# Performance work log

Measured on AMD Instinct MI355X. Metric: run time of the kernel, lower is better.

The kernel has to match this reference:

```python
import jax, jax.numpy as jnp
import numpy as np

B, N, E, H, D = 64, 500, 128, 8, 16  # batch, pomo==graph size, embed, heads, qkv_dim
NEG = -1e9
LOGIT_CLIP = 10.0


def setup_inputs() -> dict:
    key = jax.random.key(0)
    ks = jax.random.split(key, 10)
    enc_nodes = jax.random.normal(ks[0], (B, N, E), dtype=jnp.float32)
    enc_first = jax.random.normal(ks[1], (B, N, E), dtype=jnp.float32)
    enc_last = jax.random.normal(ks[2], (B, N, E), dtype=jnp.float32)
    mask_bits = jax.random.uniform(ks[3], (B, N, N)) < 0.2
    ninf_mask = jnp.where(mask_bits, jnp.float32(NEG), jnp.float32(0.0))
    # Linear weights (torch layout [out_features, in_features])
    sc = 1.0 / np.sqrt(E)
    Wq_first = jax.random.normal(ks[4], (H * D, E), dtype=jnp.float32) * sc
    Wq_last = jax.random.normal(ks[5], (H * D, E), dtype=jnp.float32) * sc
    Wk = jax.random.normal(ks[6], (H * D, E), dtype=jnp.float32) * sc
    Wv = jax.random.normal(ks[7], (H * D, E), dtype=jnp.float32) * sc
    Wc = jax.random.normal(ks[8], (E, H * D), dtype=jnp.float32) / np.sqrt(H * D)
    bc = jax.random.normal(ks[9], (E,), dtype=jnp.float32) * 0.01
    return {"encoded_nodes": enc_nodes, "encoded_first_node": enc_first,
            "encoded_last_node": enc_last, "ninf_mask": ninf_mask,
            "Wq_first": Wq_first, "Wq_last": Wq_last, "Wk": Wk, "Wv": Wv,
            "Wc": Wc, "bc": bc}


def _heads(x, W):
    # x: [B, n, E], W: [H*D, E] -> [B, H, n, D]
    y = jnp.einsum('bne,fe->bnf', x, W)
    return y.reshape(x.shape[0], x.shape[1], H, D).transpose(0, 2, 1, 3)


def reference(encoded_nodes, encoded_first_node, encoded_last_node, ninf_mask,
              Wq_first, Wq_last, Wk, Wv, Wc, bc):
    # set_q1 + Wq_last projection, summed per POMO decoder
    q = _heads(encoded_first_node, Wq_first) + _heads(encoded_last_node, Wq_last)  # [B,H,N,D]
    k = _heads(encoded_nodes, Wk)  # [B,H,N,D]
    v = _heads(encoded_nodes, Wv)  # [B,H,N,D]
    # masked multi-head attention
    score = jnp.einsum('bhnd,bhgd->bhng', q, k) / jnp.sqrt(jnp.float32(D))
    score = score + ninf_mask[:, None, :, :]
    w = jax.nn.softmax(score, axis=-1)
    out = jnp.einsum('bhng,bhgd->bhnd', w, v)  # [B,H,N,D]
    out_concat = out.transpose(0, 2, 1, 3).reshape(B, N, H * D)
    mh = jnp.einsum('bnf,ef->bne', out_concat, Wc) + bc  # multi_head_combine
    # single-head pointer attention with tanh clipping
    s = jnp.einsum('bne,bge->bng', mh, encoded_nodes) / jnp.sqrt(jnp.float32(E))
    s = LOGIT_CLIP * jnp.tanh(s) + ninf_mask
    probs = jax.nn.softmax(s, axis=2)
    return probs
```

## Files before the change

kernel.cpp:

```cpp
#include <hip/hip_runtime.h>


#define B_ 64
#define N_ 500

typedef short bf16x8 __attribute__((ext_vector_type(8)));
typedef float f32x16 __attribute__((ext_vector_type(16)));
typedef unsigned short ushort8 __attribute__((ext_vector_type(8)));

__device__ __forceinline__ float4 ld4(const float* p) { return *reinterpret_cast<const float4*>(p); }
__device__ __forceinline__ void st4(float* p, const float4 v) { *reinterpret_cast<float4*>(p) = v; }

__device__ __forceinline__ float fast_tanh(float x) {
    const float e = __expf(2.f * x);
    return 1.f - 2.f / (e + 1.f);
}

__device__ __forceinline__ unsigned short f2bf_rn(float x) {
    unsigned u = __float_as_uint(x);
    return (unsigned short)((u + 0x7FFFu + ((u >> 16) & 1u)) >> 16);
}
__device__ __forceinline__ float bf2f(unsigned short h) {
    return __uint_as_float(((unsigned)h) << 16);
}

__global__ __launch_bounds__(256) void gemm_mfma(
    const float* __restrict__ A1, const float* __restrict__ W1a, const float* __restrict__ W1b,
    const float* __restrict__ A2, const float* __restrict__ W2a, const float* __restrict__ W2b,
    const float* __restrict__ bias, float* __restrict__ C, const int F, const int nterm)
{
    __shared__ unsigned short Ah[64 * 128];
    __shared__ unsigned short Al[64 * 128];
    __shared__ unsigned short Wh[64 * 128];
    __shared__ unsigned short Wl[64 * 128];

    const int t  = threadIdx.x;
    const int rb = blockIdx.y * 64;
    const int fb = blockIdx.x * 64;
    const int l  = t & 63;
    const int w  = t >> 6;
    const int half = l >> 5;
    const int mrow = 32 * (w >> 1) + (l & 31);
    const int ncol = 32 * (w & 1) + (l & 31);

    const int sr  = t >> 2;
    const int sc0 = (t & 3) * 32;

    f32x16 acc;
#pragma unroll
    for (int i = 0; i < 16; ++i) acc[i] = 0.f;

    for (int tt = 0; tt < nterm; ++tt) {
        const float* A  = tt ? A2 : A1;
        const float* Wa = tt ? W2a : W1a;
        const float* Wb = tt ? W2b : W1b;
        const float* W  = (fb < 128) ? Wa : Wb;
        const int frbase = fb & 127;

        if (tt) __syncthreads();

#pragma unroll
        for (int it = 0; it < 4; ++it) {
            const int c = sc0 + it * 8;
            const int chunk = c >> 3;
            const int dstA = sr * 128 + ((chunk ^ (sr & 7)) << 3);
            {
                const float4 v0 = ld4(&A[(size_t)(rb + sr) * 128 + c]);
                const float4 v1 = ld4(&A[(size_t)(rb + sr) * 128 + c + 4]);
                const float f[8] = {v0.x, v0.y, v0.z, v0.w, v1.x, v1.y, v1.z, v1.w};
                ushort8 hi, lo;
#pragma unroll
                for (int e = 0; e < 8; ++e) {
                    const unsigned short h = f2bf_rn(f[e]);
                    hi[e] = h;
                    lo[e] = f2bf_rn(f[e] - bf2f(h));
                }
                *reinterpret_cast<ushort8*>(&Ah[dstA]) = hi;
                *reinterpret_cast<ushort8*>(&Al[dstA]) = lo;
            }
            {
                const float4 v0 = ld4(&W[(size_t)(frbase + sr) * 128 + c]);
                const float4 v1 = ld4(&W[(size_t)(frbase + sr) * 128 + c + 4]);
                const float f[8] = {v0.x, v0.y, v0.z, v0.w, v1.x, v1.y, v1.z, v1.w};
                ushort8 hi, lo;
#pragma unroll
                for (int e = 0; e < 8; ++e) {
                    const unsigned short h = f2bf_rn(f[e]);
                    hi[e] = h;
                    lo[e] = f2bf_rn(f[e] - bf2f(h));
                }
                *reinterpret_cast<ushort8*>(&Wh[dstA]) = hi;
                *reinterpret_cast<ushort8*>(&Wl[dstA]) = lo;
            }
        }
        __syncthreads();

#pragma unroll
        for (int ks = 0; ks < 8; ++ks) {
            const int chA = (2 * ks + half) ^ (mrow & 7);
            const int chW = (2 * ks + half) ^ (ncol & 7);
            const bf16x8 ah = *reinterpret_cast<const bf16x8*>(&Ah[mrow * 128 + chA * 8]);
            const bf16x8 al = *reinterpret_cast<const bf16x8*>(&Al[mrow * 128 + chA * 8]);
            const bf16x8 wh = *reinterpret_cast<const bf16x8*>(&Wh[ncol * 128 + chW * 8]);
            const bf16x8 wl = *reinterpret_cast<const bf16x8*>(&Wl[ncol * 128 + chW * 8]);
            acc = __builtin_amdgcn_mfma_f32_32x32x16_bf16(ah, wh, acc, 0, 0, 0);
            acc = __builtin_amdgcn_mfma_f32_32x32x16_bf16(ah, wl, acc, 0, 0, 0);
            acc = __builtin_amdgcn_mfma_f32_32x32x16_bf16(al, wh, acc, 0, 0, 0);
        }
    }

    const int col = fb + ncol;
    const float bv = bias ? bias[col] : 0.f;
#pragma unroll
    for (int r = 0; r < 16; ++r) {
        const int row = rb + 32 * (w >> 1) + (r & 3) + 8 * (r >> 2) + 4 * half;
        C[(size_t)row * F + col] = acc[r] + bv;
    }
}

__global__ __launch_bounds__(256) void attn_kernel(
    const float* __restrict__ q, const float* __restrict__ kv,
    const float* __restrict__ mask, float* __restrict__ att)
{
    __shared__ __align__(16) float Qt[16][68];
    __shared__ __align__(16) float Kt[16][68];
    __shared__ __align__(16) float Vt[16][68];
    const int t = threadIdx.x;
    const int lane = t & 63;
    const int rt = blockIdx.x;
    const int h  = blockIdx.y;
    const int b  = blockIdx.z;
    const int tr = t >> 4;
    const int jq = (t >> 2) & 3;
    const int dg = t & 3;
    const int r0 = tr * 4;
    const int srow = t >> 2;
    const int sde  = (t & 3) * 4;
    const int vswz = srow ^ (4 * (t & 3));

    {
        const int rg = min(rt * 64 + srow, 499);
        const float4 qa = ld4(&q[((size_t)(b * N_ + rg)) * 128 + h * 16 + sde]);
        Qt[sde + 0][srow] = qa.x; Qt[sde + 1][srow] = qa.y;
        Qt[sde + 2][srow] = qa.z; Qt[sde + 3][srow] = qa.w;
    }

    float out[4][4];
#pragma unroll
    for (int i = 0; i < 4; ++i)
#pragma unroll
        for (int dd = 0; dd < 4; ++dd) out[i][dd] = 0.f;
    float sum[4] = {0.f, 0.f, 0.f, 0.f};

    float4 kreg, vreg;
    {
        const int jg = min(srow, 499);
        const float* kp = &kv[((size_t)(b * N_ + jg)) * 256 + h * 16 + sde];
        kreg = ld4(kp); vreg = ld4(kp + 128);
    }

    for (int jc = 0; jc < 8; ++jc) {
        __syncthreads();
        Kt[sde + 0][srow] = kreg.x; Kt[sde + 1][srow] = kreg.y;
        Kt[sde + 2][srow] = kreg.z; Kt[sde + 3][srow] = kreg.w;
        Vt[sde + 0][vswz] = vreg.x; Vt[sde + 1][vswz] = vreg.y;
        Vt[sde + 2][vswz] = vreg.z; Vt[sde + 3][vswz] = vreg.w;
        __syncthreads();
        if (jc < 7) {
            const int jg = min(jc * 64 + 64 + srow, 499);
            const float* kp = &kv[((size_t)(b * N_ + jg)) * 256 + h * 16 + sde];
            kreg = ld4(kp); vreg = ld4(kp + 128);
        }

        const int jloc = jq * 16 + dg * 4;
        float s[4][4];
#pragma unroll
        for (int i = 0; i < 4; ++i)
#pragma unroll
            for (int j = 0; j < 4; ++j) s[i][j] = 0.f;
#pragma unroll
        for (int d = 0; d < 16; ++d) {
            const float4 a4 = ld4(&Qt[d][r0]);
            const float4 k4 = ld4(&Kt[d][jloc]);
            const float a[4] = {a4.x, a4.y, a4.z, a4.w};
            const float k[4] = {k4.x, k4.y, k4.z, k4.w};
#pragma unroll
            for (int i = 0; i < 4; ++i)
#pragma unroll
                for (int j = 0; j < 4; ++j) s[i][j] += a[i] * k[j];
        }

        const int jbase = jc * 64 + jloc;
        float p[4][4];
#pragma unroll
        for (int i = 0; i < 4; ++i) {
            const int rgc = min(rt * 64 + r0 + i, 499);
            float4 mv;
            if (jbase < 500) mv = ld4(&mask[((size_t)b * N_ + rgc) * N_ + jbase]);
            else mv = make_float4(-1e9f, -1e9f, -1e9f, -1e9f);
            p[i][0] = __expf(s[i][0] * 0.25f + mv.x);
            p[i][1] = __expf(s[i][1] * 0.25f + mv.y);
            p[i][2] = __expf(s[i][2] * 0.25f + mv.z);
            p[i][3] = __expf(s[i][3] * 0.25f + mv.w);
            sum[i] += p[i][0] + p[i][1] + p[i][2] + p[i][3];
        }

#pragma unroll
        for (int g = 0; g < 4; ++g) {
            const int sl = (lane & ~3) | g;
            const int jb = jq * 16 + 4 * (g ^ dg);
            float4 vt[4];
#pragma unroll
            for (int dd = 0; dd < 4; ++dd) vt[dd] = ld4(&Vt[dg * 4 + dd][jb]);
#pragma unroll
            for (int i = 0; i < 4; ++i) {
                const float pg0 = __shfl(p[i][0], sl, 64);
                const float pg1 = __shfl(p[i][1], sl, 64);
                const float pg2 = __shfl(p[i][2], sl, 64);
                const float pg3 = __shfl(p[i][3], sl, 64);
#pragma unroll
                for (int dd = 0; dd < 4; ++dd)
                    out[i][dd] += pg0 * vt[dd].x + pg1 * vt[dd].y
                                + pg2 * vt[dd].z + pg3 * vt[dd].w;
            }
        }
    }

#pragma unroll
    for (int m = 1; m <= 8; m <<= 1)
#pragma unroll
        for (int i = 0; i < 4; ++i) sum[i] += __shfl_xor(sum[i], m, 64);
#pragma unroll
    for (int m = 4; m <= 8; m <<= 1)
#pragma unroll
        for (int i = 0; i < 4; ++i)
#pragma unroll
            for (int dd = 0; dd < 4; ++dd) out[i][dd] += __shfl_xor(out[i][dd], m, 64);

    if (jq == 0) {
#pragma unroll
        for (int i = 0; i < 4; ++i) {
            const int rg = rt * 64 + r0 + i;
            if (rg < 500) {
                const float inv = 1.f / sum[i];
                float4 o;
                o.x = out[i][0] * inv; o.y = out[i][1] * inv;
                o.z = out[i][2] * inv; o.w = out[i][3] * inv;
                st4(&att[((size_t)(b * N_ + rg)) * 128 + h * 16 + dg * 4], o);
            }
        }
    }
}

__global__ __launch_bounds__(256) void pointer_kernel(
    const float* __restrict__ mh, const float* __restrict__ enc,
    const float* __restrict__ mask, float* __restrict__ outp)
{
    __shared__ __align__(16) float Mt[16][68];
    __shared__ __align__(16) float Et[16][68];
    const int t = threadIdx.x;
    const int rt = blockIdx.x;
    const int b  = blockIdx.y;
    const int tj = t & 15;
    const int r0 = (t >> 4) * 4;
    const int g0 = tj * 4;
    const int srow = t >> 2;
    const int sde  = (t & 3) * 4;

    int rgl = rt * 64 + srow; if (rgl > 499) rgl = 499;
    float rs[4] = {0.f, 0.f, 0.f, 0.f};

    for (int gc = 0; gc < 8; ++gc) {
        float s[4][4];
#pragma unroll
        for (int i = 0; i < 4; ++i)
#pragma unroll
            for (int j = 0; j < 4; ++j) s[i][j] = 0.f;

        for (int ec = 0; ec < 8; ++ec) {
            __syncthreads();
            const float4 mv4 = ld4(&mh[((size_t)(b * N_ + rgl)) * 128 + ec * 16 + sde]);
            Mt[sde + 0][srow] = mv4.x; Mt[sde + 1][srow] = mv4.y;
            Mt[sde + 2][srow] = mv4.z; Mt[sde + 3][srow] = mv4.w;
            int gg = gc * 64 + srow; if (gg > 499) gg = 499;
            const float4 ev = ld4(&enc[((size_t)(b * N_ + gg)) * 128 + ec * 16 + sde]);
            Et[sde + 0][srow] = ev.x; Et[sde + 1][srow] = ev.y;
            Et[sde + 2][srow] = ev.z; Et[sde + 3][srow] = ev.w;
            __syncthreads();
#pragma unroll
            for (int d = 0; d < 16; ++d) {
                const float4 a4 = ld4(&Mt[d][r0]);
                const float4 e4 = ld4(&Et[d][g0]);
                const float a[4] = {a4.x, a4.y, a4.z, a4.w};
                const float e[4] = {e4.x, e4.y, e4.z, e4.w};
#pragma unroll
                for (int i = 0; i < 4; ++i)
#pragma unroll
                    for (int j = 0; j < 4; ++j) s[i][j] += a[i] * e[j];
            }
        }

#pragma unroll
        for (int i = 0; i < 4; ++i) {
            const int rg = rt * 64 + r0 + i;
            const int gg = gc * 64 + g0;
            const bool ok = (rg < 500) && (gg < 500);
            float4 mv;
            if (ok) mv = ld4(&mask[((size_t)b * N_ + rg) * N_ + gg]);
            else mv = make_float4(-1e9f, -1e9f, -1e9f, -1e9f);
            const float c = 0.08838834764831845f;
            float4 pv;
            pv.x = __expf(10.f * fast_tanh(s[i][0] * c) + mv.x);
            pv.y = __expf(10.f * fast_tanh(s[i][1] * c) + mv.y);
            pv.z = __expf(10.f * fast_tanh(s[i][2] * c) + mv.z);
            pv.w = __expf(10.f * fast_tanh(s[i][3] * c) + mv.w);
            rs[i] += pv.x + pv.y + pv.z + pv.w;
            if (ok) st4(&outp[((size_t)b * N_ + rg) * N_ + gg], pv);
        }
    }

#pragma unroll
    for (int m = 1; m < 16; m <<= 1)
#pragma unroll
        for (int i = 0; i < 4; ++i) rs[i] += __shfl_xor(rs[i], m, 64);

    float inv[4];
#pragma unroll
    for (int i = 0; i < 4; ++i) inv[i] = 1.f / rs[i];
    for (int gc = 0; gc < 8; ++gc) {
#pragma unroll
        for (int i = 0; i < 4; ++i) {
            const int rg = rt * 64 + r0 + i;
            const int gg = gc * 64 + g0;
            if (rg < 500 && gg < 500) {
                float* pp = &outp[((size_t)b * N_ + rg) * N_ + gg];
                float4 v = ld4(pp);
                v.x *= inv[i]; v.y *= inv[i]; v.z *= inv[i]; v.w *= inv[i];
                st4(pp, v);
            }
        }
    }
}

extern "C" void kernel_launch(void* const* d_in, const int* in_sizes, int n_in,
                              void* d_out, int out_size, void* d_ws, size_t ws_size,
                              hipStream_t stream) {
    const float* enc  = (const float*)d_in[0];
    const float* encf = (const float*)d_in[1];
    const float* encl = (const float*)d_in[2];
    const float* mask = (const float*)d_in[3];
    const float* Wqf  = (const float*)d_in[4];
    const float* Wql  = (const float*)d_in[5];
    const float* Wk   = (const float*)d_in[6];
    const float* Wv   = (const float*)d_in[7];
    const float* Wc   = (const float*)d_in[8];
    const float* bc   = (const float*)d_in[9];
    float* out = (float*)d_out;
    float* ws = (float*)d_ws;

    float* ws_q    = ws;
    float* ws_kv   = ws + 4096000;
    float* ws_att  = ws + 12288000;
    float* ws_mh   = ws_q;

    gemm_mfma<<<dim3(2, 500), 256, 0, stream>>>(encf, Wqf, nullptr, encl, Wql, nullptr,
                                                nullptr, ws_q, 128, 2);
    gemm_mfma<<<dim3(4, 500), 256, 0, stream>>>(enc, Wk, Wv, nullptr, nullptr, nullptr,
                                                nullptr, ws_kv, 256, 1);
    attn_kernel<<<dim3(8, 8, 64), 256, 0, stream>>>(ws_q, ws_kv, mask, ws_att);
    gemm_mfma<<<dim3(2, 500), 256, 0, stream>>>(ws_att, Wc, nullptr, nullptr, nullptr, nullptr,
                                                bc, ws_mh, 128, 1);
    pointer_kernel<<<dim3(8, 64), 256, 0, stream>>>(ws_mh, enc, mask, out);
}
```

Baseline: 538.7 us.

## Move masked attention onto bf16x3 MFMA and pack float mask into bitmask

Replaces the FP32 FMA-based attention kernel with an MFMA version that splits Q, K, V and the probabilities into bf16 hi/lo pairs (three-term products) and uses permlane32 swaps to reshape score fragments into A operands. A new pre-pass packs the float additive mask into a per-row bitmask stored temporarily in the output buffer, so each attention block (eight heads per row) reads bits instead of re-reading the full float mask. This cuts the mask bandwidth and the scalar FMA load, at the cost of an extra kernel launch, bf16 split conversions in the inner loop, and reliance on the output buffer being overwritten later by the pointer kernel.

```diff
diff --git a/kernel.cpp b/kernel.cpp
--- a/kernel.cpp
+++ b/kernel.cpp
@@ -7,6 +7,7 @@
 typedef short bf16x8 __attribute__((ext_vector_type(8)));
 typedef float f32x16 __attribute__((ext_vector_type(16)));
 typedef unsigned short ushort8 __attribute__((ext_vector_type(8)));
+typedef unsigned uint2v __attribute__((ext_vector_type(2)));
 
 __device__ __forceinline__ float4 ld4(const float* p) { return *reinterpret_cast<const float4*>(p); }
 __device__ __forceinline__ void st4(float* p, const float4 v) { *reinterpret_cast<float4*>(p) = v; }
@@ -15,13 +16,34 @@
     const float e = __expf(2.f * x);
     return 1.f - 2.f / (e + 1.f);
 }
-
 __device__ __forceinline__ unsigned short f2bf_rn(float x) {
     unsigned u = __float_as_uint(x);
     return (unsigned short)((u + 0x7FFFu + ((u >> 16) & 1u)) >> 16);
 }
 __device__ __forceinline__ float bf2f(unsigned short h) {
     return __uint_as_float(((unsigned)h) << 16);
+}
+__device__ __forceinline__ unsigned cvt_pk_bf16(float lo, float hi) {
+    unsigned r;
+    asm("v_cvt_pk_bf16_f32 %0, %1, %2" : "=v"(r) : "v"(lo), "v"(hi));
+    return r;
+}
+
+__global__ __launch_bounds__(256) void mask_pack(
+    const float* __restrict__ mask, unsigned long long* __restrict__ bits)
+{
+    const int w = threadIdx.x >> 6, l = threadIdx.x & 63;
+    const int n = blockIdx.x * 4 + w;
+    const int b = blockIdx.y;
+    const float* mrow = &mask[((size_t)b * N_ + n) * N_];
+    unsigned long long* brow = &bits[((size_t)b * N_ + n) * 8];
+#pragma unroll
+    for (int c = 0; c < 8; ++c) {
+        const int j = c * 64 + l;
+        const bool pred = (j >= N_) || (mrow[min(j, N_ - 1)] < -1.f);
+        const unsigned long long bal = __ballot(pred);
+        if (l == 0) brow[c] = bal;
+    }
 }
 
 __global__ __launch_bounds__(256) void gemm_mfma(
@@ -42,7 +64,6 @@
     const int half = l >> 5;
     const int mrow = 32 * (w >> 1) + (l & 31);
     const int ncol = 32 * (w & 1) + (l & 31);
-
     const int sr  = t >> 2;
     const int sc0 = (t & 3) * 32;
 
@@ -118,136 +139,144 @@
     }
 }
 
-__global__ __launch_bounds__(256) void attn_kernel(
+__global__ __launch_bounds__(256) void attn_mfma(
     const float* __restrict__ q, const float* __restrict__ kv,
-    const float* __restrict__ mask, float* __restrict__ att)
+    const unsigned* __restrict__ bits, float* __restrict__ att)
 {
-    __shared__ __align__(16) float Qt[16][68];
-    __shared__ __align__(16) float Kt[16][68];
-    __shared__ __align__(16) float Vt[16][68];
-    const int t = threadIdx.x;
-    const int lane = t & 63;
+    __shared__ __align__(16) unsigned short Kh[32 * 16];
+    __shared__ __align__(16) unsigned short Kl[32 * 16];
+    __shared__ __align__(16) unsigned short Vh[32 * 40];
+    __shared__ __align__(16) unsigned short Vl[32 * 40];
+    __shared__ float Rinv[4][32];
+
+    const int t  = threadIdx.x;
+    const int w  = t >> 6;
+    const int l  = t & 63;
+    const int lr = l & 31;
+    const int h  = l >> 5;
     const int rt = blockIdx.x;
-    const int h  = blockIdx.y;
+    const int hh = blockIdx.y;
     const int b  = blockIdx.z;
-    const int tr = t >> 4;
-    const int jq = (t >> 2) & 3;
-    const int dg = t & 3;
-    const int r0 = tr * 4;
-    const int srow = t >> 2;
-    const int sde  = (t & 3) * 4;
-    const int vswz = srow ^ (4 * (t & 3));
-
+
+    const int r_base = rt * 128 + w * 32;
+    const int rc = min(r_base + lr, N_ - 1);
+
+    bf16x8 qh, ql;
     {
-        const int rg = min(rt * 64 + srow, 499);
-        const float4 qa = ld4(&q[((size_t)(b * N_ + rg)) * 128 + h * 16 + sde]);
-        Qt[sde + 0][srow] = qa.x; Qt[sde + 1][srow] = qa.y;
-        Qt[sde + 2][srow] = qa.z; Qt[sde + 3][srow] = qa.w;
-    }
-
-    float out[4][4];
-#pragma unroll
-    for (int i = 0; i < 4; ++i)
-#pragma unroll
-        for (int dd = 0; dd < 4; ++dd) out[i][dd] = 0.f;
-    float sum[4] = {0.f, 0.f, 0.f, 0.f};
-
-    float4 kreg, vreg;
-    {
-        const int jg = min(srow, 499);
-        const float* kp = &kv[((size_t)(b * N_ + jg)) * 256 + h * 16 + sde];
-        kreg = ld4(kp); vreg = ld4(kp + 128);
-    }
-
-    for (int jc = 0; jc < 8; ++jc) {
+        const float* qp = &q[((size_t)(b * N_ + rc)) * 128 + hh * 16 + 8 * h];
+        const float4 a = ld4(qp), c = ld4(qp + 4);
+        const float f[8] = {a.x, a.y, a.z, a.w, c.x, c.y, c.z, c.w};
+#pragma unroll
+        for (int e = 0; e < 8; ++e) {
+            const float v = f[e] * 0.25f;
+            const unsigned short hi = f2bf_rn(v);
+            qh[e] = (short)hi;
+            ql[e] = (short)f2bf_rn(v - bf2f(hi));
+        }
+    }
+
+    const int sj   = t >> 3;
+    const int sd   = (t & 7) * 2;
+    const int kswz = sd ^ (8 * ((sj >> 2) & 1));
+    const int vd   = t & 15;
+    const int vj2  = (t >> 4) * 2;
+
+    const f32x16 z = {0.f};
+    f32x16 out;
+#pragma unroll
+    for (int i = 0; i < 16; ++i) out[i] = 0.f;
+    float rowsum = 0.f;
+
+    const unsigned* brow = &bits[(size_t)(b * N_ + rc) * 16];
+    const int kchunk = h ^ ((lr >> 2) & 1);
+
+    for (int js = 0; js < 16; ++js) {
+        const int j0 = js * 32;
         __syncthreads();
-        Kt[sde + 0][srow] = kreg.x; Kt[sde + 1][srow] = kreg.y;
-        Kt[sde + 2][srow] = kreg.z; Kt[sde + 3][srow] = kreg.w;
-        Vt[sde + 0][vswz] = vreg.x; Vt[sde + 1][vswz] = vreg.y;
-        Vt[sde + 2][vswz] = vreg.z; Vt[sde + 3][vswz] = vreg.w;
+        {
+            const int jg = min(j0 + sj, N_ - 1);
+            const float2 kk = *reinterpret_cast<const float2*>(
+                &kv[((size_t)(b * N_ + jg)) * 256 + hh * 16 + sd]);
+            const unsigned short h0 = f2bf_rn(kk.x), h1 = f2bf_rn(kk.y);
+            const unsigned short l0 = f2bf_rn(kk.x - bf2f(h0)), l1 = f2bf_rn(kk.y - bf2f(h1));
+            *reinterpret_cast<unsigned*>(&Kh[sj * 16 + kswz]) = (unsigned)h0 | ((unsigned)h1 << 16);
+            *reinterpret_cast<unsigned*>(&Kl[sj * 16 + kswz]) = (unsigned)l0 | ((unsigned)l1 << 16);
+        }
+        {
+            const int jg0 = min(j0 + vj2, N_ - 1), jg1 = min(j0 + vj2 + 1, N_ - 1);
+            const float v0 = kv[((size_t)(b * N_ + jg0)) * 256 + 128 + hh * 16 + vd];
+            const float v1 = kv[((size_t)(b * N_ + jg1)) * 256 + 128 + hh * 16 + vd];
+            const unsigned short h0 = f2bf_rn(v0), h1 = f2bf_rn(v1);
+            const unsigned short l0 = f2bf_rn(v0 - bf2f(h0)), l1 = f2bf_rn(v1 - bf2f(h1));
+            *reinterpret_cast<unsigned*>(&Vh[vd * 40 + vj2]) = (unsigned)h0 | ((unsigned)h1 << 16);
+            *reinterpret_cast<unsigned*>(&Vl[vd * 40 + vj2]) = (unsigned)l0 | ((unsigned)l1 << 16);
+        }
         __syncthreads();
-        if (jc < 7) {
-            const int jg = min(jc * 64 + 64 + srow, 499);
-            const float* kp = &kv[((size_t)(b * N_ + jg)) * 256 + h * 16 + sde];
-            kreg = ld4(kp); vreg = ld4(kp + 128);
-        }
-
-        const int jloc = jq * 16 + dg * 4;
-        float s[4][4];
-#pragma unroll
-        for (int i = 0; i < 4; ++i)
-#pragma unroll
-            for (int j = 0; j < 4; ++j) s[i][j] = 0.f;
-#pragma unroll
-        for (int d = 0; d < 16; ++d) {
-            const float4 a4 = ld4(&Qt[d][r0]);
-            const float4 k4 = ld4(&Kt[d][jloc]);
-            const float a[4] = {a4.x, a4.y, a4.z, a4.w};
-            const float k[4] = {k4.x, k4.y, k4.z, k4.w};
-#pragma unroll
-            for (int i = 0; i < 4; ++i)
-#pragma unroll
-                for (int j = 0; j < 4; ++j) s[i][j] += a[i] * k[j];
-        }
-
-        const int jbase = jc * 64 + jloc;
-        float p[4][4];
-#pragma unroll
-        for (int i = 0; i < 4; ++i) {
-            const int rgc = min(rt * 64 + r0 + i, 499);
-            float4 mv;
-            if (jbase < 500) mv = ld4(&mask[((size_t)b * N_ + rgc) * N_ + jbase]);
-            else mv = make_float4(-1e9f, -1e9f, -1e9f, -1e9f);
-            p[i][0] = __expf(s[i][0] * 0.25f + mv.x);
-            p[i][1] = __expf(s[i][1] * 0.25f + mv.y);
-            p[i][2] = __expf(s[i][2] * 0.25f + mv.z);
-            p[i][3] = __expf(s[i][3] * 0.25f + mv.w);
-            sum[i] += p[i][0] + p[i][1] + p[i][2] + p[i][3];
-        }
-
-#pragma unroll
-        for (int g = 0; g < 4; ++g) {
-            const int sl = (lane & ~3) | g;
-            const int jb = jq * 16 + 4 * (g ^ dg);
-            float4 vt[4];
-#pragma unroll
-            for (int dd = 0; dd < 4; ++dd) vt[dd] = ld4(&Vt[dg * 4 + dd][jb]);
-#pragma unroll
-            for (int i = 0; i < 4; ++i) {
-                const float pg0 = __shfl(p[i][0], sl, 64);
-                const float pg1 = __shfl(p[i][1], sl, 64);
-                const float pg2 = __shfl(p[i][2], sl, 64);
-                const float pg3 = __shfl(p[i][3], sl, 64);
-#pragma unroll
-                for (int dd = 0; dd < 4; ++dd)
-                    out[i][dd] += pg0 * vt[dd].x + pg1 * vt[dd].y
-                                + pg2 * vt[dd].z + pg3 * vt[dd].w;
-            }
-        }
-    }
-
-#pragma unroll
-    for (int m = 1; m <= 8; m <<= 1)
-#pragma unroll
-        for (int i = 0; i < 4; ++i) sum[i] += __shfl_xor(sum[i], m, 64);
-#pragma unroll
-    for (int m = 4; m <= 8; m <<= 1)
-#pragma unroll
-        for (int i = 0; i < 4; ++i)
-#pragma unroll
-            for (int dd = 0; dd < 4; ++dd) out[i][dd] += __shfl_xor(out[i][dd], m, 64);
-
-    if (jq == 0) {
-#pragma unroll
-        for (int i = 0; i < 4; ++i) {
-            const int rg = rt * 64 + r0 + i;
-            if (rg < 500) {
-                const float inv = 1.f / sum[i];
-                float4 o;
-                o.x = out[i][0] * inv; o.y = out[i][1] * inv;
-                o.z = out[i][2] * inv; o.w = out[i][3] * inv;
-                st4(&att[((size_t)(b * N_ + rg)) * 128 + h * 16 + dg * 4], o);
-            }
+
+        const bf16x8 kfh = *reinterpret_cast<const bf16x8*>(&Kh[lr * 16 + kchunk * 8]);
+        const bf16x8 kfl = *reinterpret_cast<const bf16x8*>(&Kl[lr * 16 + kchunk * 8]);
+        f32x16 st = __builtin_amdgcn_mfma_f32_32x32x16_bf16(kfh, qh, z, 0, 0, 0);
+        st = __builtin_amdgcn_mfma_f32_32x32x16_bf16(kfh, ql, st, 0, 0, 0);
+        st = __builtin_amdgcn_mfma_f32_32x32x16_bf16(kfl, qh, st, 0, 0, 0);
+
+        const unsigned bw = brow[js];
+        float p[16];
+#pragma unroll
+        for (int g = 0; g < 16; ++g) {
+            const int crow = (g & 3) + 8 * (g >> 2) + 4 * h;
+            const float e = __expf(st[g]);
+            p[g] = ((bw >> crow) & 1u) ? 0.f : e;
+            rowsum += p[g];
+        }
+
+        unsigned wH[8], wL[8];
+#pragma unroll
+        for (int i = 0; i < 8; ++i) {
+            wH[i] = cvt_pk_bf16(p[2 * i], p[2 * i + 1]);
+            const float r0 = p[2 * i]     - __uint_as_float(wH[i] << 16);
+            const float r1 = p[2 * i + 1] - __uint_as_float(wH[i] & 0xffff0000u);
+            wL[i] = cvt_pk_bf16(r0, r1);
+        }
+
+        const uint2v aH0 = __builtin_amdgcn_permlane32_swap(wH[0], wH[2], false, false);
+        const uint2v bH0 = __builtin_amdgcn_permlane32_swap(wH[1], wH[3], false, false);
+        const uint2v aH1 = __builtin_amdgcn_permlane32_swap(wH[4], wH[6], false, false);
+        const uint2v bH1 = __builtin_amdgcn_permlane32_swap(wH[5], wH[7], false, false);
+        const uint2v aL0 = __builtin_amdgcn_permlane32_swap(wL[0], wL[2], false, false);
+        const uint2v bL0 = __builtin_amdgcn_permlane32_swap(wL[1], wL[3], false, false);
+        const uint2v aL1 = __builtin_amdgcn_permlane32_swap(wL[4], wL[6], false, false);
+        const uint2v bL1 = __builtin_amdgcn_permlane32_swap(wL[5], wL[7], false, false);
+        union { unsigned u[4]; bf16x8 v; } pH0 = {{aH0[0], bH0[0], aH0[1], bH0[1]}};
+        union { unsigned u[4]; bf16x8 v; } pH1 = {{aH1[0], bH1[0], aH1[1], bH1[1]}};
+        union { unsigned u[4]; bf16x8 v; } pL0 = {{aL0[0], bL0[0], aL0[1], bL0[1]}};
+        union { unsigned u[4]; bf16x8 v; } pL1 = {{aL1[0], bL1[0], aL1[1], bL1[1]}};
+
+        const bf16x8 vh0 = *reinterpret_cast<const bf16x8*>(&Vh[lr * 40 + 0 * 16 + 8 * h]);
+        const bf16x8 vl0 = *reinterpret_cast<const bf16x8*>(&Vl[lr * 40 + 0 * 16 + 8 * h]);
+        const bf16x8 vh1 = *reinterpret_cast<const bf16x8*>(&Vh[lr * 40 + 1 * 16 + 8 * h]);
+        const bf16x8 vl1 = *reinterpret_cast<const bf16x8*>(&Vl[lr * 40 + 1 * 16 + 8 * h]);
+        out = __builtin_amdgcn_mfma_f32_32x32x16_bf16(pH0.v, vh0, out, 0, 0, 0);
+        out = __builtin_amdgcn_mfma_f32_32x32x16_bf16(pL0.v, vh0, out, 0, 0, 0);
+        out = __builtin_amdgcn_mfma_f32_32x32x16_bf16(pH0.v, vl0, out, 0, 0, 0);
+        out = __builtin_amdgcn_mfma_f32_32x32x16_bf16(pH1.v, vh1, out, 0, 0, 0);
+        out = __builtin_amdgcn_mfma_f32_32x32x16_bf16(pL1.v, vh1, out, 0, 0, 0);
+        out = __builtin_amdgcn_mfma_f32_32x32x16_bf16(pH1.v, vl1, out, 0, 0, 0);
+    }
+
+    rowsum += __shfl_xor(rowsum, 32, 64);
+    if (h == 0) Rinv[w][lr] = 1.f / rowsum;
+    const float4 i0 = *reinterpret_cast<const float4*>(&Rinv[w][4 * h]);
+    const float4 i1 = *reinterpret_cast<const float4*>(&Rinv[w][8 + 4 * h]);
+    const float4 i2 = *reinterpret_cast<const float4*>(&Rinv[w][16 + 4 * h]);
+    const float4 i3 = *reinterpret_cast<const float4*>(&Rinv[w][24 + 4 * h]);
+    const float iv[16] = {i0.x, i0.y, i0.z, i0.w, i1.x, i1.y, i1.z, i1.w,
+                          i2.x, i2.y, i2.z, i2.w, i3.x, i3.y, i3.z, i3.w};
+    if (lr < 16) {
+#pragma unroll
+        for (int g = 0; g < 16; ++g) {
+            const int row = r_base + (g & 3) + 8 * (g >> 2) + 4 * h;
+            if (row < N_)
+                att[((size_t)(b * N_ + row)) * 128 + hh * 16 + lr] = out[g] * iv[g];
         }
     }
 }
@@ -363,11 +392,14 @@
     float* ws_att  = ws + 12288000;
     float* ws_mh   = ws_q;
 
+    unsigned long long* bits64 = (unsigned long long*)d_out;
+
+    mask_pack<<<dim3(125, 64), 256, 0, stream>>>(mask, bits64);
     gemm_mfma<<<dim3(2, 500), 256, 0, stream>>>(encf, Wqf, nullptr, encl, Wql, nullptr,
                                                 nullptr, ws_q, 128, 2);
     gemm_mfma<<<dim3(4, 500), 256, 0, stream>>>(enc, Wk, Wv, nullptr, nullptr, nullptr,
                                                 nullptr, ws_kv, 256, 1);
-    attn_kernel<<<dim3(8, 8, 64), 256, 0, stream>>>(ws_q, ws_kv, mask, ws_att);
+    attn_mfma<<<dim3(4, 8, 64), 256, 0, stream>>>(ws_q, ws_kv, (const unsigned*)d_out, ws_att);
     gemm_mfma<<<dim3(2, 500), 256, 0, stream>>>(ws_att, Wc, nullptr, nullptr, nullptr, nullptr,
                                                 bc, ws_mh, 128, 1);
     pointer_kernel<<<dim3(8, 64), 256, 0, stream>>>(ws_mh, enc, mask, out);
```

Measured after the change: 434.2 us. 19.4% less time.
